# Kernel tuning notes

Hardware: AMD Instinct MI355X
Metric: run time of the kernel (lower is better)

The kernel has to match this reference:

```python
import jax, jax.numpy as jnp
import numpy as np

NUM_EMBEDDINGS = 512
EMBEDDING_DIM = 128
COMMITMENT_COST = 0.25
DECAY = 0.99
EPSILON = 1e-5


def setup_inputs() -> dict:
    key = jax.random.key(0)
    k1, k2 = jax.random.split(key)
    inputs = jax.random.normal(k1, (2, EMBEDDING_DIM, 32, 32, 32), dtype=jnp.float32)
    embedding_w = jax.random.normal(k2, (NUM_EMBEDDINGS, EMBEDDING_DIM), dtype=jnp.float32)
    ema_cluster_size = jnp.zeros((NUM_EMBEDDINGS,), dtype=jnp.float32)
    ema_w = embedding_w  # buffer initialized as a clone of the codebook
    return {"inputs": inputs, "embedding_w": embedding_w,
            "ema_cluster_size": ema_cluster_size, "ema_w": ema_w}


def reference(inputs, embedding_w, ema_cluster_size, ema_w):
    B, C, D, H, W = inputs.shape
    K = embedding_w.shape[0]

    # flatten: channel-last then [N, C]
    flat_input = jnp.transpose(inputs, (0, 2, 3, 4, 1)).reshape(-1, C)  # [N, C]
    N = flat_input.shape[0]

    # squared-euclidean distances to the codebook: [N, K]
    distances = ((flat_input ** 2).sum(axis=1, keepdims=True)
                 + (embedding_w ** 2).sum(axis=1)[None, :]
                 - 2.0 * flat_input @ embedding_w.T)

    encoding_indices = jnp.argmax(-distances, axis=1)  # [N] int32

    # entropy regularizer over soft assignments (temperature 1.0)
    probs = jax.nn.softmax(-distances, axis=1)
    entropy_loss = 0.01 * (-jnp.sum(probs * jnp.log(probs + 1e-8)) / N)

    # embed: gather codebook rows, reshape to channel-first volume
    quantized_raw = embedding_w[encoding_indices].reshape(B, D, H, W, C)
    quantized_raw = jnp.transpose(quantized_raw, (0, 4, 1, 2, 3))  # [B, C, D, H, W]

    # commitment loss (codebook is EMA-updated, not grad-updated)
    commit_loss = COMMITMENT_COST * jnp.mean(
        (jax.lax.stop_gradient(quantized_raw) - inputs) ** 2)
    loss = commit_loss + entropy_loss

    # straight-through estimator output
    quantized = inputs + jax.lax.stop_gradient(quantized_raw - inputs)

    # EMA codebook update (scatter-add over argmin clusters)
    encodings_sum = jnp.zeros((K,), flat_input.dtype).at[encoding_indices].add(1.0)
    dw = jnp.zeros((K, C), flat_input.dtype).at[encoding_indices].add(flat_input)
    new_cluster_size = DECAY * ema_cluster_size + (1.0 - DECAY) * encodings_sum
    n_total = new_cluster_size.sum()
    smoothed = (new_cluster_size + EPSILON) / (n_total + K * EPSILON) * n_total
    new_ema_w = DECAY * ema_w + (1.0 - DECAY) * dw
    new_embedding_w = new_ema_w / smoothed[:, None]

    encoding_indices_vol = encoding_indices.reshape(B, D, H, W)
    return (quantized, loss, encoding_indices_vol,
            new_cluster_size, new_ema_w, new_embedding_w)
```

## Files before the change

### kernel.cpp

```cpp
#include <hip/hip_runtime.h>

#define LOSS_OFF  8388608
#define IDX_OFF   8388609
#define NCS_OFF   8454145
#define EMAW_OFF  8454657
#define EMB_OFF   8520193

typedef __attribute__((ext_vector_type(8))) short short8;
typedef __attribute__((ext_vector_type(4))) float f32x4;

#define LOG2E 1.4426950408889634f
#define N2L2E -2.8853900817779268f
#define LN2   0.6931471805599453f
#define NSPLIT 32

__device__ __forceinline__ unsigned short bf16r(float x) {
  unsigned u = __float_as_uint(x);
  u += 0x7fff + ((u >> 16) & 1);
  return (unsigned short)(u >> 16);
}
__device__ __forceinline__ float bf16tof(unsigned short h) {
  return __uint_as_float(((unsigned)h) << 16);
}

__global__ __launch_bounds__(256) void prep_kernel(const float* __restrict__ emb,
    unsigned short* __restrict__ ehig, unsigned short* __restrict__ elog,
    float* __restrict__ eeg)
{
  __shared__ float r1[256];
  const int t = threadIdx.x;
  const int k = blockIdx.x * 2 + (t >> 7);
  const int c = t & 127;
  float x = emb[k * 128 + c];
  unsigned short hh = bf16r(x);
  ehig[k * 128 + c] = hh;
  elog[k * 128 + c] = bf16r(x - bf16tof(hh));
  r1[t] = x * x;
  __syncthreads();
  #pragma unroll
  for (int off = 64; off; off >>= 1) {
    if ((t & 127) < off) r1[t] += r1[t + off];
    __syncthreads();
  }
  if ((t & 127) == 0) eeg[k] = LOG2E * r1[t];
}

__global__ __attribute__((amdgpu_flat_work_group_size(256, 256),
                          amdgpu_waves_per_eu(2, 4)))
void dist_kernel(const float* __restrict__ inputs,
                 const unsigned short* __restrict__ ehig,
                 const unsigned short* __restrict__ elog,
                 const float* __restrict__ eeg,
                 float* __restrict__ out, float* __restrict__ idxws,
                 float* __restrict__ sums)
{
  __shared__ __align__(16) short esm[2][2][32 * 136];
  __shared__ float eeL[512];
  __shared__ float xxs[64];
  __shared__ float red[8];
  float* xs = (float*)&esm[0][0][0];

  const int t = threadIdx.x, lane = t & 63, wave = t >> 6;
  const int n0 = blockIdx.x * 64;
  const int b = n0 >> 15, s0 = n0 & 32767;
  const int col = lane & 15, quad = lane >> 4;
  const int kk = t >> 3, c0s = (t & 7) * 16;

  eeL[t] = eeg[t]; eeL[256 + t] = eeg[256 + t];

  short8 ahi[4], alo[4];
  for (int r4 = 0; r4 < 2; ++r4) {
    __syncthreads();
    {
      const int rr = t & 31, cc = (t >> 5) * 16;
      const float* src = inputs + (size_t)b * 128 * 32768 + s0 + r4 * 32 + rr;
      #pragma unroll
      for (int i = 0; i < 16; ++i)
        xs[rr * 132 + cc + i] = src[(size_t)(cc + i) * 32768];
    }
    __syncthreads();
    if ((wave >> 1) == r4) {
      float xacc = 0.f;
      const float* xr = &xs[((wave & 1) * 16 + col) * 132 + quad * 8];
      #pragma unroll
      for (int q = 0; q < 4; ++q) {
        float v[8];
        *(float4*)&v[0] = *(const float4*)(xr + q * 32);
        *(float4*)&v[4] = *(const float4*)(xr + q * 32 + 4);
        short8 h8, l8;
        #pragma unroll
        for (int j = 0; j < 8; ++j) {
          unsigned short hh = bf16r(v[j]);
          h8[j] = (short)hh;
          l8[j] = (short)bf16r(v[j] - bf16tof(hh));
          xacc += v[j] * v[j];
        }
        ahi[q] = h8; alo[q] = l8;
      }
      xacc += __shfl_xor(xacc, 16);
      xacc += __shfl_xor(xacc, 32);
      if (quad == 0) xxs[wave * 16 + col] = xacc;
    }
  }
  __syncthreads();

  uint4 ph0, ph1, pl0, pl1;
  {
    const size_t go = (size_t)kk * 128 + c0s;
    ph0 = ((const uint4*)(ehig + go))[0]; ph1 = ((const uint4*)(ehig + go))[1];
    pl0 = ((const uint4*)(elog + go))[0]; pl1 = ((const uint4*)(elog + go))[1];
  }
  *(uint4*)&esm[0][0][kk * 136 + c0s] = ph0;
  *(uint4*)&esm[0][0][kk * 136 + c0s + 8] = ph1;
  *(uint4*)&esm[0][1][kk * 136 + c0s] = pl0;
  *(uint4*)&esm[0][1][kk * 136 + c0s + 8] = pl1;
  {
    const size_t go = (size_t)(32 + kk) * 128 + c0s;
    ph0 = ((const uint4*)(ehig + go))[0]; ph1 = ((const uint4*)(ehig + go))[1];
    pl0 = ((const uint4*)(elog + go))[0]; pl1 = ((const uint4*)(elog + go))[1];
  }

  float mS[4], sS[4], tS[4]; int kS[4];
  #pragma unroll
  for (int i = 0; i < 4; ++i) { mS[i] = 1e30f; sS[i] = 0.f; tS[i] = 0.f; kS[i] = 0; }

  for (int st = 0; st < 16; ++st) {
    const int pb = st & 1;
    __syncthreads();
    #pragma unroll
    for (int kt = 0; kt < 2; ++kt) {
      f32x4 ac = {0.f, 0.f, 0.f, 0.f};
      const int boff = (kt * 16 + col) * 136 + quad * 8;
      #pragma unroll
      for (int q = 0; q < 4; ++q) {
        short8 bh = *(const short8*)&esm[pb][0][boff + q * 32];
        short8 bl = *(const short8*)&esm[pb][1][boff + q * 32];
        ac = __builtin_amdgcn_mfma_f32_16x16x32_bf16(alo[q], bh, ac, 0, 0, 0);
        ac = __builtin_amdgcn_mfma_f32_16x16x32_bf16(ahi[q], bl, ac, 0, 0, 0);
        ac = __builtin_amdgcn_mfma_f32_16x16x32_bf16(ahi[q], bh, ac, 0, 0, 0);
      }
      const int code = st * 32 + kt * 16 + col;
      const float eec2 = eeL[code];
      #pragma unroll
      for (int si = 0; si < 4; ++si) {
        float d  = fmaf(ac[si], N2L2E, eec2);
        float mo = mS[si];
        float mn = fminf(mo, d);
        float mx = fmaxf(mo, d);
        float E  = __builtin_amdgcn_exp2f(mn - mx);
        bool nw  = d < mo;
        float f  = nw ? E : 1.f;
        float e2 = nw ? 1.f : E;
        tS[si] = (tS[si] + (mn - mo) * sS[si]) * f + (mn - d) * e2;
        sS[si] = sS[si] * f + e2;
        kS[si] = nw ? code : kS[si];
        mS[si] = mn;
      }
    }
    if (st < 15) {
      const int nb = pb ^ 1;
      *(uint4*)&esm[nb][0][kk * 136 + c0s] = ph0;
      *(uint4*)&esm[nb][0][kk * 136 + c0s + 8] = ph1;
      *(uint4*)&esm[nb][1][kk * 136 + c0s] = pl0;
      *(uint4*)&esm[nb][1][kk * 136 + c0s + 8] = pl1;
      if (st < 14) {
        const size_t go = (size_t)((st + 2) * 32 + kk) * 128 + c0s;
        ph0 = ((const uint4*)(ehig + go))[0]; ph1 = ((const uint4*)(ehig + go))[1];
        pl0 = ((const uint4*)(elog + go))[0]; pl1 = ((const uint4*)(elog + go))[1];
      }
    }
  }

  #pragma unroll
  for (int off = 1; off <= 8; off <<= 1) {
    #pragma unroll
    for (int si = 0; si < 4; ++si) {
      float m2 = __shfl_xor(mS[si], off);
      float S2 = __shfl_xor(sS[si], off);
      float T2 = __shfl_xor(tS[si], off);
      int   k2 = __shfl_xor(kS[si], off);
      float mo = mS[si];
      float mn = fminf(mo, m2);
      float f1 = __builtin_amdgcn_exp2f(mn - mo);
      float f2 = __builtin_amdgcn_exp2f(mn - m2);
      tS[si] = (tS[si] + (mn - mo) * sS[si]) * f1 + (T2 + (mn - m2) * S2) * f2;
      sS[si] = sS[si] * f1 + S2 * f2;
      if (m2 < mo || (m2 == mo && k2 < kS[si])) kS[si] = k2;
      mS[si] = mn;
    }
  }

  float cacc = 0.f, eacc = 0.f;
  if (col == 0) {
    #pragma unroll
    for (int si = 0; si < 4; ++si) {
      int row = wave * 16 + quad * 4 + si;
      int rn = n0 + row;
      float fk = (float)kS[si];
      out[IDX_OFF + rn] = fk;
      idxws[rn] = fk;
      cacc += xxs[row] + mS[si] * LN2;
      eacc += LN2 * (tS[si] / sS[si] - __builtin_amdgcn_logf(sS[si]));
    }
  }
  cacc += __shfl_xor(cacc, 16); cacc += __shfl_xor(cacc, 32);
  eacc += __shfl_xor(eacc, 16); eacc += __shfl_xor(eacc, 32);
  if (lane == 0) { red[wave] = cacc; red[4 + wave] = eacc; }
  __syncthreads();
  if (t == 0) {
    unsafeAtomicAdd(&sums[0], red[0] + red[1] + red[2] + red[3]);
    unsafeAtomicAdd(&sums[1], red[4] + red[5] + red[6] + red[7]);
  }
}

__global__ __launch_bounds__(256) void scatter_kernel(
    const float* __restrict__ inputs, const float* __restrict__ idxws,
    float* partial, float* __restrict__ cpart)
{
  __shared__ float acc[512 * 9];
  __shared__ float cnts[512];
  const int t = threadIdx.x;
  const int s = blockIdx.x >> 4, ccB = blockIdx.x & 15;
  const int R = 65536 / NSPLIT;
  for (int m = t; m < 512 * 9; m += 256) acc[m] = 0.f;
  if (ccB == 0) for (int m = t; m < 512; m += 256) cnts[m] = 0.f;
  __syncthreads();
  const int l = t & 63, cg = t >> 6;
  for (int it = 0; it < R / 256; ++it) {
    int n = s * R + it * 256;
    int bb = n >> 15;
    int sp = (n & 32767) + 4 * l;
    float4 i4 = *(const float4*)(idxws + n + 4 * l);
    int k0 = (int)i4.x, k1 = (int)i4.y, k2 = (int)i4.z, k3 = (int)i4.w;
    #pragma unroll
    for (int ci = 0; ci < 2; ++ci) {
      int c = cg * 2 + ci;
      float4 x4 = *(const float4*)(inputs + ((size_t)bb * 128 + ccB * 8 + c) * 32768 + sp);
      atomicAdd(&acc[k0 * 9 + c], x4.x);
      atomicAdd(&acc[k1 * 9 + c], x4.y);
      atomicAdd(&acc[k2 * 9 + c], x4.z);
      atomicAdd(&acc[k3 * 9 + c], x4.w);
    }
    if (ccB == 0 && cg == 0) {
      atomicAdd(&cnts[k0], 1.f); atomicAdd(&cnts[k1], 1.f);
      atomicAdd(&cnts[k2], 1.f); atomicAdd(&cnts[k3], 1.f);
    }
  }
  __syncthreads();
  for (int m = t; m < 512 * 8; m += 256) {
    int k = m >> 3, c = m & 7;
    partial[(size_t)s * 65536 + k * 128 + ccB * 8 + c] = acc[k * 9 + c];
  }
  if (ccB == 0) for (int m = t; m < 512; m += 256) cpart[s * 512 + m] = cnts[m];
}

__global__ __launch_bounds__(256) void fin_kernel(const float* __restrict__ ecs,
    const float* __restrict__ emaw, const float* partial,
    const float* __restrict__ cpart, const float* __restrict__ sums,
    float* out)
{
  __shared__ float cn[512];
  __shared__ float rsum[256];
  const int t = threadIdx.x;
  float local = 0.f;
  for (int k = t; k < 512; k += 256) {
    float c = 0.f;
    for (int s = 0; s < NSPLIT; ++s) c += cpart[s * 512 + k];
    float v = 0.99f * ecs[k] + 0.01f * c;
    cn[k] = v; local += v;
  }
  rsum[t] = local;
  __syncthreads();
  for (int o = 128; o; o >>= 1) {
    if (t < o) rsum[t] += rsum[t + o];
    __syncthreads();
  }
  const float ntot = rsum[0];
  if (blockIdx.x == 0) {
    for (int k = t; k < 512; k += 256) out[NCS_OFF + k] = cn[k];
    if (t == 0)
      out[LOSS_OFF] = 0.25f * sums[0] / 8388608.f - 0.01f * sums[1] / 65536.f;
  }
  const int i = blockIdx.x * 256 + t;
  float dwv = 0.f;
  for (int s = 0; s < NSPLIT; ++s) dwv += partial[(size_t)s * 65536 + i];
  float val = 0.99f * emaw[i] + 0.01f * dwv;
  const int k = i >> 7;
  float sm = (cn[k] + 1e-5f) / (ntot + 0.00512f) * ntot;
  out[EMAW_OFF + i] = val;
  out[EMB_OFF + i] = val / sm;
}

__global__ __launch_bounds__(256) void gather_kernel(const float* __restrict__ emb,
    const float* __restrict__ idxws, float* __restrict__ out)
{
  __shared__ float eq[128 * 64];
  const int t  = threadIdx.x;
  const int n0 = blockIdx.x * 64;
  const int b  = n0 >> 15;
  const int s0 = n0 & 32767;
  {
    const int r  = t >> 2;
    const int qq = t & 3;
    const int kidx = (int)idxws[n0 + r];
    const float* src = emb + (size_t)kidx * 128;
    #pragma unroll
    for (int i = 0; i < 8; ++i) {
      int g = qq + 4 * i;
      float4 v = *(const float4*)(src + g * 4);
      float* dst = &eq[(g * 4) * 64 + r];
      dst[0] = v.x; dst[64] = v.y; dst[128] = v.z; dst[192] = v.w;
    }
  }
  __syncthreads();
  {
    const int sl = (t & 15) * 4;
    const int cb = t >> 4;
    #pragma unroll
    for (int j = 0; j < 8; ++j) {
      int c = cb + 16 * j;
      float4 v = *(const float4*)&eq[c * 64 + sl];
      *(float4*)(out + ((size_t)b * 128 + c) * 32768 + s0 + sl) = v;
    }
  }
}

extern "C" void kernel_launch(void* const* d_in, const int* in_sizes, int n_in,
                              void* d_out, int out_size, void* d_ws, size_t ws_size,
                              hipStream_t stream) {
  const float* inputs = (const float*)d_in[0];
  const float* emb    = (const float*)d_in[1];
  const float* ecs    = (const float*)d_in[2];
  const float* emaw   = (const float*)d_in[3];
  float* out = (float*)d_out;
  float* wsf = (float*)d_ws;
  (void)in_sizes; (void)n_in; (void)out_size; (void)ws_size;

  float* idxws = wsf;
  float* sums  = wsf + 65536;
  float* eeg   = wsf + 65552;
  unsigned short* ehig = (unsigned short*)(wsf + 66064);
  unsigned short* elog = ehig + 65536;
  float* cpart = (float*)(elog + 65536);

  hipMemsetAsync(sums, 0, 16 * sizeof(float), stream);
  prep_kernel   <<<256,        256, 0, stream>>>(emb, ehig, elog, eeg);
  dist_kernel   <<<1024,       256, 0, stream>>>(inputs, ehig, elog, eeg, out, idxws, sums);
  scatter_kernel<<<16 * NSPLIT,256, 0, stream>>>(inputs, idxws, out, cpart);
  fin_kernel    <<<256,        256, 0, stream>>>(ecs, emaw, out, cpart, sums, out);
  gather_kernel <<<1024,       256, 0, stream>>>(emb, idxws, out);
}
```

Baseline: 199.6 us.

## Merge scatter, gather and finalize into one cooperative kernel with grid sync

Replaces the scatter, finalize and gather launches with one cooperative kernel. The first 512 blocks do the scatter-add while the other 256 blocks gather codebook rows into the quantized output, so the two phases run side by side, and a grid sync then hands off to the finalize phase. Scatter partials now go to a workspace buffer instead of the output, and the old path is kept as a fallback when the workspace is too small. This saves launch gaps and overlaps independent work, but relies on all 768 blocks being resident at once and adds the cost of a grid barrier.

```diff
diff --git a/kernel.cpp b/kernel.cpp
--- a/kernel.cpp
+++ b/kernel.cpp
@@ -1,4 +1,5 @@
 #include <hip/hip_runtime.h>
+#include <hip/hip_cooperative_groups.h>
 
 #define LOSS_OFF  8388608
 #define IDX_OFF   8388609
@@ -213,6 +214,124 @@
   }
 }
 
+__global__ __launch_bounds__(256, 4) void coop_kernel(
+    const float* __restrict__ inputs, const float* __restrict__ idxws,
+    float* __restrict__ partial, float* __restrict__ cpart,
+    const float* __restrict__ ecs, const float* __restrict__ emaw,
+    const float* __restrict__ sums, const float* __restrict__ emb,
+    float* __restrict__ out)
+{
+  __shared__ float sh[8192];
+  const int t = threadIdx.x;
+  const int bid = blockIdx.x;
+  cooperative_groups::grid_group grid = cooperative_groups::this_grid();
+
+  if (bid < 512) {
+    float* acc  = sh;
+    float* cnts = sh + 4608;
+    const int s = bid >> 4, ccB = bid & 15;
+    const int R = 65536 / NSPLIT;
+    for (int m = t; m < 4608; m += 256) acc[m] = 0.f;
+    if (ccB == 0) for (int m = t; m < 512; m += 256) cnts[m] = 0.f;
+    __syncthreads();
+    const int l = t & 63, cg = t >> 6;
+    for (int it = 0; it < R / 256; ++it) {
+      int n = s * R + it * 256;
+      int bb = n >> 15;
+      int sp = (n & 32767) + 4 * l;
+      float4 i4 = *(const float4*)(idxws + n + 4 * l);
+      int k0 = (int)i4.x, k1 = (int)i4.y, k2 = (int)i4.z, k3 = (int)i4.w;
+      #pragma unroll
+      for (int ci = 0; ci < 2; ++ci) {
+        int c = cg * 2 + ci;
+        float4 x4 = *(const float4*)(inputs + ((size_t)bb * 128 + ccB * 8 + c) * 32768 + sp);
+        atomicAdd(&acc[k0 * 9 + c], x4.x);
+        atomicAdd(&acc[k1 * 9 + c], x4.y);
+        atomicAdd(&acc[k2 * 9 + c], x4.z);
+        atomicAdd(&acc[k3 * 9 + c], x4.w);
+      }
+      if (ccB == 0 && cg == 0) {
+        atomicAdd(&cnts[k0], 1.f); atomicAdd(&cnts[k1], 1.f);
+        atomicAdd(&cnts[k2], 1.f); atomicAdd(&cnts[k3], 1.f);
+      }
+    }
+    __syncthreads();
+    for (int m = t; m < 512 * 8; m += 256) {
+      int k = m >> 3, c = m & 7;
+      partial[(size_t)s * 65536 + k * 128 + ccB * 8 + c] = acc[k * 9 + c];
+    }
+    if (ccB == 0) for (int m = t; m < 512; m += 256) cpart[s * 512 + m] = cnts[m];
+  } else {
+    float* eq = sh;
+    for (int rd = 0; rd < 4; ++rd) {
+      const int n0 = (bid - 512) * 256 + rd * 64;
+      const int b  = n0 >> 15;
+      const int s0 = n0 & 32767;
+      __syncthreads();
+      {
+        const int r  = t >> 2;
+        const int qq = t & 3;
+        const int kidx = (int)idxws[n0 + r];
+        const float* src = emb + (size_t)kidx * 128;
+        #pragma unroll
+        for (int i = 0; i < 8; ++i) {
+          int g = qq + 4 * i;
+          float4 v = *(const float4*)(src + g * 4);
+          float* dst = &eq[(g * 4) * 64 + r];
+          dst[0] = v.x; dst[64] = v.y; dst[128] = v.z; dst[192] = v.w;
+        }
+      }
+      __syncthreads();
+      {
+        const int sl = (t & 15) * 4;
+        const int cb = t >> 4;
+        #pragma unroll
+        for (int j = 0; j < 8; ++j) {
+          int c = cb + 16 * j;
+          float4 v = *(const float4*)&eq[c * 64 + sl];
+          *(float4*)(out + ((size_t)b * 128 + c) * 32768 + s0 + sl) = v;
+        }
+      }
+    }
+  }
+
+  __threadfence();
+  grid.sync();
+
+  if (bid < 256) {
+    float* cn   = sh;
+    float* rsum = sh + 512;
+    __syncthreads();
+    float local = 0.f;
+    for (int k = t; k < 512; k += 256) {
+      float c = 0.f;
+      for (int s = 0; s < NSPLIT; ++s) c += cpart[s * 512 + k];
+      float v = 0.99f * ecs[k] + 0.01f * c;
+      cn[k] = v; local += v;
+    }
+    rsum[t] = local;
+    __syncthreads();
+    for (int o = 128; o; o >>= 1) {
+      if (t < o) rsum[t] += rsum[t + o];
+      __syncthreads();
+    }
+    const float ntot = rsum[0];
+    if (bid == 0) {
+      for (int k = t; k < 512; k += 256) out[NCS_OFF + k] = cn[k];
+      if (t == 0)
+        out[LOSS_OFF] = 0.25f * sums[0] / 8388608.f - 0.01f * sums[1] / 65536.f;
+    }
+    const int i = bid * 256 + t;
+    float dwv = 0.f;
+    for (int s = 0; s < NSPLIT; ++s) dwv += partial[(size_t)s * 65536 + i];
+    float val = 0.99f * emaw[i] + 0.01f * dwv;
+    const int k = i >> 7;
+    float sm = (cn[k] + 1e-5f) / (ntot + 0.00512f) * ntot;
+    out[EMAW_OFF + i] = val;
+    out[EMB_OFF + i] = val / sm;
+  }
+}
+
 __global__ __launch_bounds__(256) void scatter_kernel(
     const float* __restrict__ inputs, const float* __restrict__ idxws,
     float* partial, float* __restrict__ cpart)
@@ -334,7 +453,7 @@
   const float* emaw   = (const float*)d_in[3];
   float* out = (float*)d_out;
   float* wsf = (float*)d_ws;
-  (void)in_sizes; (void)n_in; (void)out_size; (void)ws_size;
+  (void)in_sizes; (void)n_in; (void)out_size;
 
   float* idxws = wsf;
   float* sums  = wsf + 65536;
@@ -342,11 +461,24 @@
   unsigned short* ehig = (unsigned short*)(wsf + 66064);
   unsigned short* elog = ehig + 65536;
   float* cpart = (float*)(elog + 65536);
+  float* partial = cpart + 16384;
+  const size_t need = ((size_t)(partial - wsf) + (size_t)NSPLIT * 65536) * 4;
+  const bool big = ws_size >= need;
 
   hipMemsetAsync(sums, 0, 16 * sizeof(float), stream);
-  prep_kernel   <<<256,        256, 0, stream>>>(emb, ehig, elog, eeg);
-  dist_kernel   <<<1024,       256, 0, stream>>>(inputs, ehig, elog, eeg, out, idxws, sums);
-  scatter_kernel<<<16 * NSPLIT,256, 0, stream>>>(inputs, idxws, out, cpart);
-  fin_kernel    <<<256,        256, 0, stream>>>(ecs, emaw, out, cpart, sums, out);
-  gather_kernel <<<1024,       256, 0, stream>>>(emb, idxws, out);
-}
+  prep_kernel<<<256,  256, 0, stream>>>(emb, ehig, elog, eeg);
+  dist_kernel<<<1024, 256, 0, stream>>>(inputs, ehig, elog, eeg, out, idxws, sums);
+
+  if (big) {
+    void* kargs[] = { (void*)&inputs, (void*)&idxws, (void*)&partial,
+                      (void*)&cpart, (void*)&ecs, (void*)&emaw,
+                      (void*)&sums, (void*)&emb, (void*)&out };
+    hipLaunchCooperativeKernel((const void*)coop_kernel, dim3(768), dim3(256),
+                               kargs, 0, stream);
+  } else {
+    float* pout = out;
+    scatter_kernel<<<16 * NSPLIT, 256, 0, stream>>>(inputs, idxws, pout, cpart);
+    fin_kernel    <<<256,         256, 0, stream>>>(ecs, emaw, pout, cpart, sums, out);
+    gather_kernel <<<1024,        256, 0, stream>>>(emb, idxws, out);
+  }
+}
```

Result: slower. 389.5 us (+95.1%).
